# Performance work log

Hardware: AMD Instinct MI355X
Metric: run time of the kernel (lower is better)

## Reference

```python
import jax, jax.numpy as jnp
import numpy as np

# --- HairBundle model constants (from init_kwargs: params + force_params) ---
# Nadrowski/Martin-style hair-bundle model with 5 state variables:
#   x_hb (bundle position), x_a (adaptation motor), p_m, p_gs, p_t (Ca probs)
LAM    = 1.0    # bundle friction
LAM_A  = 10.0   # adaptation-motor friction
K_GS   = 0.75   # gating-spring stiffness
K_SP   = 0.6    # stereociliary-pivot stiffness
K_ES   = 0.45   # extent spring stiffness
D_GATE = 0.5    # gating swing
DELTA  = 0.25   # channel sensitivity length
F_MAX  = 0.35   # max motor force
S_CA   = 0.9    # Ca feedback strength on motors
C_M    = 1.2    # Ca binding rate (motor site)
K_M    = 0.8    # Ca unbinding rate (motor site)
TAU_M  = 1.0
C_GS   = 0.7    # Ca binding rate (gating-spring site)
K_GSR  = 0.5    # Ca unbinding rate (gating-spring site)
TAU_GS = 1.0
C_T    = 0.3    # Ca binding rate (transduction site)
K_T    = 0.4    # Ca unbinding rate (transduction site)
TAU_T  = 1.0
HB_NOISE = 0.05 # diffusion on x_hb
A_NOISE  = 0.02 # diffusion on x_a
# force_params: sinusoidal driving force
F_AMP   = 0.5
F_OMEGA = 6.283185307179586
F_PHASE = 0.0

BATCH = 8_000_000  # number of SDE sample paths
NVARS = 5


def setup_inputs() -> dict:
    key = jax.random.key(0)
    k1, k2 = jax.random.split(key)
    t = jax.random.uniform(k1, (1,), dtype=jnp.float32)
    x = jax.random.normal(k2, (BATCH, NVARS), dtype=jnp.float32)
    return {"t": t, "x": x}


def reference(t, x):
    """Vectorized drift f(t, x) of the hair-bundle SDE (replaces the
    per-row python loop + sympy lambdified scalar evaluation) plus the
    constant diagonal diffusion g(t, x). Returns (drift, diffusion)."""
    x_hb, x_a, p_m, p_gs, p_t = (x[..., 0], x[..., 1], x[..., 2], x[..., 3], x[..., 4])

    # channel open probability and gating-spring force (elementwise, fused)
    p_o = jax.nn.sigmoid((x_hb - x_a) / DELTA)          # [B]
    f_gs = K_GS * (x_hb - x_a - D_GATE * p_o)           # [B]

    force = F_AMP * jnp.sin(F_OMEGA * t[0] + F_PHASE)   # scalar sin drive, added to dx_hb

    dx_hb = (-f_gs - K_SP * x_hb) / LAM + force
    dx_a  = (f_gs - K_ES * x_a - F_MAX * (1.0 - S_CA * p_m)) / LAM_A
    dp_m  = (C_M * p_o * (1.0 - p_m) - K_M * p_m) / TAU_M
    dp_gs = (C_GS * p_o * (1.0 - p_gs) - K_GSR * p_gs) / TAU_GS
    dp_t  = (C_T * p_o * (1.0 - p_t) - K_T * p_t) / TAU_T

    drift = jnp.stack([dx_hb, dx_a, dp_m, dp_gs, dp_t], axis=-1)  # [B, 5]

    # g: constant per-variable noise amplitudes tiled over the batch
    dsigma = jnp.array([HB_NOISE, A_NOISE, 0.0, 0.0, 0.0], dtype=x.dtype)
    diffusion = jnp.broadcast_to(dsigma, x.shape)  # [B, 5]

    return drift, diffusion
```

## Files before the change

### kernel.cpp

```cpp
#include <hip/hip_runtime.h>
#include <math.h>


typedef float f4 __attribute__((ext_vector_type(4)));

#define THREADS        128
#define ROWS_PER_BLOCK 512
#define F4_PER_BLOCK   (ROWS_PER_BLOCK * 5 / 4)
#define F4_PER_THREAD  (F4_PER_BLOCK / THREADS)
#define ROWS_PER_THREAD (ROWS_PER_BLOCK / THREADS)

__global__ __launch_bounds__(THREADS) void hb_sde_kernel(
    const float* __restrict__ t,
    const float* __restrict__ x,
    float* __restrict__ drift,
    float* __restrict__ diff)
{
    __shared__ float lds[ROWS_PER_BLOCK * 5];

    const int i = threadIdx.x;
    const long long f4base = (long long)blockIdx.x * F4_PER_BLOCK;

    const float force = 0.5f * sinf(6.283185307179586f * t[0]);

    const f4* __restrict__ xv = (const f4*)x + f4base;
    f4* lv = (f4*)lds;
#pragma unroll
    for (int k = 0; k < F4_PER_THREAD; ++k)
        lv[i + k * THREADS] = __builtin_nontemporal_load(&xv[i + k * THREADS]);
    __syncthreads();

#pragma unroll
    for (int r = 0; r < ROWS_PER_THREAD; ++r) {
        const int o = (i * ROWS_PER_THREAD + r) * 5;
        const float x_hb = lds[o + 0];
        const float x_a  = lds[o + 1];
        const float p_m  = lds[o + 2];
        const float p_gs = lds[o + 3];
        const float p_t  = lds[o + 4];

        const float p_o  = 1.0f / (1.0f + __expf(-4.0f * (x_hb - x_a)));
        const float f_gs = 0.75f * (x_hb - x_a - 0.5f * p_o);

        lds[o + 0] = -f_gs - 0.6f * x_hb + force;
        lds[o + 1] = 0.1f * (f_gs - 0.45f * x_a - 0.35f * (1.0f - 0.9f * p_m));
        lds[o + 2] = 1.2f * p_o * (1.0f - p_m)  - 0.8f * p_m;
        lds[o + 3] = 0.7f * p_o * (1.0f - p_gs) - 0.5f * p_gs;
        lds[o + 4] = 0.3f * p_o * (1.0f - p_t)  - 0.4f * p_t;
    }
    __syncthreads();

    f4* __restrict__ dv = (f4*)drift + f4base;
#pragma unroll
    for (int k = 0; k < F4_PER_THREAD; ++k)
        __builtin_nontemporal_store(lv[i + k * THREADS], &dv[i + k * THREADS]);

    f4* __restrict__ gv = (f4*)diff + f4base;
#pragma unroll
    for (int k = 0; k < F4_PER_THREAD; ++k) {
        const int m = (i + k * THREADS) % 5;
        f4 v;
        v.x = (m == 0) ? 0.05f : ((m == 4) ? 0.02f : 0.0f);
        v.y = (m == 0) ? 0.02f : ((m == 1) ? 0.05f : 0.0f);
        v.z = (m == 1) ? 0.02f : ((m == 2) ? 0.05f : 0.0f);
        v.w = (m == 2) ? 0.02f : ((m == 3) ? 0.05f : 0.0f);
        __builtin_nontemporal_store(v, &gv[i + k * THREADS]);
    }
}

extern "C" void kernel_launch(void* const* d_in, const int* in_sizes, int n_in,
                              void* d_out, int out_size, void* d_ws, size_t ws_size,
                              hipStream_t stream) {
    const float* t = (const float*)d_in[0];
    const float* x = (const float*)d_in[1];
    float* out = (float*)d_out;

    const long long batch = (long long)in_sizes[1] / 5;
    float* drift = out;
    float* diff  = out + batch * 5;

    const int nblocks = (int)(batch / ROWS_PER_BLOCK);
    hb_sde_kernel<<<nblocks, THREADS, 0, stream>>>(t, x, drift, diff);
}
```

Baseline: 411.5 us.

## Replace LDS staging with per-thread contiguous register loads of four rows

Each thread now loads five consecutive float4 values, which hold four complete rows, straight into registers. It computes the drift there and stores it directly, so the shared-memory staging and both __syncthreads barriers are gone. The diffusion pattern becomes five fixed constant vectors with no modulo selection. Nontemporal load and store hints are dropped. The cost is that per-thread strided 80-byte chunks give less coalescing than the earlier interleaved float4 access, and the cache behaviour for this streaming data changes.

```diff
diff --git a/kernel.cpp b/kernel.cpp
--- a/kernel.cpp
+++ b/kernel.cpp
@@ -4,11 +4,21 @@
 
 typedef float f4 __attribute__((ext_vector_type(4)));
 
-#define THREADS        128
-#define ROWS_PER_BLOCK 512
-#define F4_PER_BLOCK   (ROWS_PER_BLOCK * 5 / 4)
-#define F4_PER_THREAD  (F4_PER_BLOCK / THREADS)
-#define ROWS_PER_THREAD (ROWS_PER_BLOCK / THREADS)
+#define THREADS         128
+#define ROWS_PER_THREAD 4
+#define ROWS_PER_BLOCK  (THREADS * ROWS_PER_THREAD)
+#define F4_PER_THREAD   5
+
+#define HB_ROW(xhb, xa, pm, pgs, pt, o0, o1, o2, o3, o4)                 \
+    do {                                                                 \
+        const float p_o  = 1.0f / (1.0f + __expf(-4.0f * ((xhb) - (xa)))); \
+        const float f_gs = 0.75f * ((xhb) - (xa) - 0.5f * p_o);          \
+        (o0) = -f_gs - 0.6f * (xhb) + force;                             \
+        (o1) = 0.1f * (f_gs - 0.45f * (xa) - 0.35f * (1.0f - 0.9f * (pm))); \
+        (o2) = 1.2f * p_o * (1.0f - (pm))  - 0.8f * (pm);                \
+        (o3) = 0.7f * p_o * (1.0f - (pgs)) - 0.5f * (pgs);               \
+        (o4) = 0.3f * p_o * (1.0f - (pt))  - 0.4f * (pt);                \
+    } while (0)
 
 __global__ __launch_bounds__(THREADS) void hb_sde_kernel(
     const float* __restrict__ t,
@@ -16,56 +26,38 @@
     float* __restrict__ drift,
     float* __restrict__ diff)
 {
-    __shared__ float lds[ROWS_PER_BLOCK * 5];
+    const int i = threadIdx.x;
+    const long long tf4 =
+        (long long)blockIdx.x * (ROWS_PER_BLOCK * 5 / 4) + (long long)i * F4_PER_THREAD;
 
-    const int i = threadIdx.x;
-    const long long f4base = (long long)blockIdx.x * F4_PER_BLOCK;
+    const f4* __restrict__ xv = (const f4*)x + tf4;
+    const f4 a0 = xv[0];
+    const f4 a1 = xv[1];
+    const f4 a2 = xv[2];
+    const f4 a3 = xv[3];
+    const f4 a4 = xv[4];
 
     const float force = 0.5f * sinf(6.283185307179586f * t[0]);
 
-    const f4* __restrict__ xv = (const f4*)x + f4base;
-    f4* lv = (f4*)lds;
-#pragma unroll
-    for (int k = 0; k < F4_PER_THREAD; ++k)
-        lv[i + k * THREADS] = __builtin_nontemporal_load(&xv[i + k * THREADS]);
-    __syncthreads();
+    f4 d0, d1, d2, d3, d4;
+    HB_ROW(a0.x,  a0.y,  a0.z,  a0.w,  a1.x,   d0.x,  d0.y,  d0.z,  d0.w,  d1.x);
+    HB_ROW(a1.y,  a1.z,  a1.w,  a2.x,  a2.y,   d1.y,  d1.z,  d1.w,  d2.x,  d2.y);
+    HB_ROW(a2.z,  a2.w,  a3.x,  a3.y,  a3.z,   d2.z,  d2.w,  d3.x,  d3.y,  d3.z);
+    HB_ROW(a3.w,  a4.x,  a4.y,  a4.z,  a4.w,   d3.w,  d4.x,  d4.y,  d4.z,  d4.w);
 
-#pragma unroll
-    for (int r = 0; r < ROWS_PER_THREAD; ++r) {
-        const int o = (i * ROWS_PER_THREAD + r) * 5;
-        const float x_hb = lds[o + 0];
-        const float x_a  = lds[o + 1];
-        const float p_m  = lds[o + 2];
-        const float p_gs = lds[o + 3];
-        const float p_t  = lds[o + 4];
+    f4* __restrict__ dv = (f4*)drift + tf4;
+    dv[0] = d0;
+    dv[1] = d1;
+    dv[2] = d2;
+    dv[3] = d3;
+    dv[4] = d4;
 
-        const float p_o  = 1.0f / (1.0f + __expf(-4.0f * (x_hb - x_a)));
-        const float f_gs = 0.75f * (x_hb - x_a - 0.5f * p_o);
-
-        lds[o + 0] = -f_gs - 0.6f * x_hb + force;
-        lds[o + 1] = 0.1f * (f_gs - 0.45f * x_a - 0.35f * (1.0f - 0.9f * p_m));
-        lds[o + 2] = 1.2f * p_o * (1.0f - p_m)  - 0.8f * p_m;
-        lds[o + 3] = 0.7f * p_o * (1.0f - p_gs) - 0.5f * p_gs;
-        lds[o + 4] = 0.3f * p_o * (1.0f - p_t)  - 0.4f * p_t;
-    }
-    __syncthreads();
-
-    f4* __restrict__ dv = (f4*)drift + f4base;
-#pragma unroll
-    for (int k = 0; k < F4_PER_THREAD; ++k)
-        __builtin_nontemporal_store(lv[i + k * THREADS], &dv[i + k * THREADS]);
-
-    f4* __restrict__ gv = (f4*)diff + f4base;
-#pragma unroll
-    for (int k = 0; k < F4_PER_THREAD; ++k) {
-        const int m = (i + k * THREADS) % 5;
-        f4 v;
-        v.x = (m == 0) ? 0.05f : ((m == 4) ? 0.02f : 0.0f);
-        v.y = (m == 0) ? 0.02f : ((m == 1) ? 0.05f : 0.0f);
-        v.z = (m == 1) ? 0.02f : ((m == 2) ? 0.05f : 0.0f);
-        v.w = (m == 2) ? 0.02f : ((m == 3) ? 0.05f : 0.0f);
-        __builtin_nontemporal_store(v, &gv[i + k * THREADS]);
-    }
+    f4* __restrict__ gv = (f4*)diff + tf4;
+    gv[0] = (f4){0.05f, 0.02f, 0.0f,  0.0f };
+    gv[1] = (f4){0.0f,  0.05f, 0.02f, 0.0f };
+    gv[2] = (f4){0.0f,  0.0f,  0.05f, 0.02f};
+    gv[3] = (f4){0.0f,  0.0f,  0.0f,  0.05f};
+    gv[4] = (f4){0.02f, 0.0f,  0.0f,  0.0f };
 }
 
 extern "C" void kernel_launch(void* const* d_in, const int* in_sizes, int n_in,
```

Measured after the change: 449.6 us. 9.3% more time.
